# Optimization experiments

Hardware: AMD Instinct MI355X
Metric: run time of the kernel (lower is better)

## Reference

```python
import jax, jax.numpy as jnp
import numpy as np

EPS = 1e-5
B, S, P = 2, 512, 4096
TD, SD, H, ED = 512, 384, 8, 32
HD = TD // H


def _ln(x, g, b):
    m = jnp.mean(x, axis=-1, keepdims=True)
    v = jnp.var(x, axis=-1, keepdims=True)
    return (x - m) * jax.lax.rsqrt(v + EPS) * g + b


def setup_inputs() -> dict:
    key = jax.random.key(0)
    ks = iter(jax.random.split(key, 24))

    def lin(din, dout):
        W = jax.random.normal(next(ks), (din, dout), jnp.float32) / np.sqrt(din)
        b = jnp.zeros((dout,), jnp.float32)
        return W, b

    Wq, bq = lin(TD, TD)
    Wk, bk = lin(SD, TD)
    Wv, bv = lin(SD, TD)
    Wo, bo = lin(TD, TD)
    W1, b1 = lin(TD, 4 * TD)
    W2, b2 = lin(4 * TD, TD)
    edge_emb = jax.random.normal(next(ks), (H, ED), jnp.float32)
    ep_w = jax.random.normal(next(ks), (ED,), jnp.float32) / np.sqrt(ED)
    ep_b = jnp.zeros((), jnp.float32)

    return dict(
        text_features=jax.random.normal(next(ks), (B, S, TD), jnp.float32),
        shape_features=jax.random.normal(next(ks), (B, P, SD), jnp.float32),
        tn_g=jnp.ones((TD,), jnp.float32), tn_b=jnp.zeros((TD,), jnp.float32),
        sn_g=jnp.ones((SD,), jnp.float32), sn_b=jnp.zeros((SD,), jnp.float32),
        Wq=Wq, bq=bq, Wk=Wk, bk=bk, Wv=Wv, bv=bv,
        edge_emb=edge_emb, ep_w=ep_w, ep_b=ep_b,
        Wo=Wo, bo=bo,
        on_g=jnp.ones((TD,), jnp.float32), on_b=jnp.zeros((TD,), jnp.float32),
        W1=W1, b1=b1, W2=W2, b2=b2,
        fn_g=jnp.ones((TD,), jnp.float32), fn_b=jnp.zeros((TD,), jnp.float32),
    )


def reference(text_features, shape_features, tn_g, tn_b, sn_g, sn_b,
              Wq, bq, Wk, bk, Wv, bv, edge_emb, ep_w, ep_b, Wo, bo,
              on_g, on_b, W1, b1, W2, b2, fn_g, fn_b):
    b, n, _ = text_features.shape
    tn = _ln(text_features, tn_g, tn_b)
    sn = _ln(shape_features, sn_g, sn_b)
    residual = text_features

    # [b, h, n, d] projections
    q = (tn @ Wq + bq).reshape(b, n, H, HD).transpose(0, 2, 1, 3)
    k = (sn @ Wk + bk).reshape(b, -1, H, HD).transpose(0, 2, 1, 3)
    v = (sn @ Wv + bv).reshape(b, -1, H, HD).transpose(0, 2, 1, 3)

    scale = HD ** -0.5
    base_attn = jnp.einsum('bhid,bhjd->bhij', q, k) * scale  # [b,h,n,p]

    # edge_attn[:,h] = base_attn[:,h,:,:,None] * edge_emb[h]; then Linear(ED,1)+LeakyReLU.
    # Algebraically: score = leaky_relu(base_attn * (edge_emb @ ep_w) + ep_b)
    s = edge_emb @ ep_w  # [H] per-head scalar
    edge_scores = jax.nn.leaky_relu(base_attn * s[None, :, None, None] + ep_b, 0.2)

    attn = jax.nn.softmax(base_attn + edge_scores, axis=-1)
    out = jnp.einsum('bhij,bhjd->bhid', attn, v)
    out = out.transpose(0, 2, 1, 3).reshape(b, n, TD)
    out = out @ Wo + bo
    out = _ln(residual + out, on_g, on_b)

    ffn = jax.nn.gelu(out @ W1 + b1, approximate=False) @ W2 + b2
    out = _ln(out + ffn, fn_g, fn_b)
    return out, attn
```

## Files before the change

kernel.cpp:

```cpp
#include <hip/hip_runtime.h>
#include <math.h>

#define B_  2
#define S_  512
#define P_  4096
#define TD_ 512
#define SD_ 384
#define H_  8
#define HD_ 64
#define FF_ 2048

typedef _Float16 half8 __attribute__((ext_vector_type(8)));
typedef _Float16 half4 __attribute__((ext_vector_type(4)));
typedef float floatx4 __attribute__((ext_vector_type(4)));

__global__ __launch_bounds__(256) void wtrans_kernel(
    const float* __restrict__ src, _Float16* __restrict__ dst, int K, int N)
{
    __shared__ float ts[32][33];
    int k0 = blockIdx.y * 32, n0 = blockIdx.x * 32;
    int tid = threadIdx.x;
#pragma unroll
    for (int i = 0; i < 4; ++i) {
        int e = i * 256 + tid;
        int kk = e >> 5, nn = e & 31;
        ts[kk][nn] = src[(size_t)(k0 + kk) * N + n0 + nn];
    }
    __syncthreads();
#pragma unroll
    for (int i = 0; i < 4; ++i) {
        int e = i * 256 + tid;
        int nn = e >> 5, kk = e & 31;
        dst[(size_t)(n0 + nn) * K + k0 + kk] = (_Float16)ts[kk][nn];
    }
}

__device__ __forceinline__ float2 block_sum2(float a, float b) {
    for (int off = 32; off > 0; off >>= 1) {
        a += __shfl_down(a, off);
        b += __shfl_down(b, off);
    }
    __shared__ float sa[8], sb[8];
    int w = threadIdx.x >> 6;
    if ((threadIdx.x & 63) == 0) { sa[w] = a; sb[w] = b; }
    __syncthreads();
    int nw = blockDim.x >> 6;
    float ta = 0.f, tb = 0.f;
    for (int i = 0; i < nw; ++i) { ta += sa[i]; tb += sb[i]; }
    __syncthreads();
    return make_float2(ta, tb);
}

__global__ __launch_bounds__(256) void ln_in_f16_kernel(
    const float* __restrict__ x, const float* __restrict__ g,
    const float* __restrict__ be, _Float16* __restrict__ yh, int D)
{
    int row = blockIdx.x;
    const float* xr = x + (size_t)row * D;
    float s = 0.f, s2 = 0.f;
    for (int i = threadIdx.x; i < D; i += 256) {
        float v = xr[i]; s += v; s2 += v * v;
    }
    float2 r = block_sum2(s, s2);
    float mean = r.x / (float)D;
    float var  = r.y / (float)D - mean * mean;
    float rstd = rsqrtf(var + 1e-5f);
    _Float16* yr = yh + (size_t)row * D;
    for (int i = threadIdx.x; i < D; i += 256)
        yr[i] = (_Float16)((xr[i] - mean) * rstd * g[i] + be[i]);
}

__global__ __launch_bounds__(256) void ln_add_kernel(
    const float* __restrict__ a, const float* __restrict__ c,
    const float* __restrict__ g, const float* __restrict__ be,
    float* __restrict__ yf, _Float16* __restrict__ yh, int D)
{
    int row = blockIdx.x;
    const float* ar = a + (size_t)row * D;
    const float* cr = c + (size_t)row * D;
    float s = 0.f, s2 = 0.f;
    for (int i = threadIdx.x; i < D; i += 256) {
        float v = ar[i] + cr[i]; s += v; s2 += v * v;
    }
    float2 rd = block_sum2(s, s2);
    float mean = rd.x / (float)D;
    float var  = rd.y / (float)D - mean * mean;
    float rstd = rsqrtf(var + 1e-5f);
    for (int i = threadIdx.x; i < D; i += 256) {
        float v = ar[i] + cr[i];
        float o = (v - mean) * rstd * g[i] + be[i];
        if (yf) yf[(size_t)row * D + i] = o;
        if (yh) yh[(size_t)row * D + i] = (_Float16)o;
    }
}

template<int ACT, int OUTF, int OUTH, int VT>
__global__ __launch_bounds__(256) void gemm_f16_kernel(
    const _Float16* __restrict__ A, const _Float16* __restrict__ Bt,
    const float* __restrict__ bias, float* __restrict__ Cf,
    _Float16* __restrict__ Ch, int M, int N, int K)
{
    __shared__ _Float16 As[128 * 40];
    __shared__ _Float16 Bs[128 * 40];
    int tid = threadIdx.x;
    int bm = blockIdx.y * 128, bn = blockIdx.x * 128;
    int wave = tid >> 6, lane = tid & 63, quad = lane >> 4, r = lane & 15;
    int mh = (wave & 1) * 64, nh = (wave >> 1) * 64;

    floatx4 acc[4][4];
    floatx4 zz = {0.f, 0.f, 0.f, 0.f};
#pragma unroll
    for (int i = 0; i < 4; ++i)
#pragma unroll
        for (int j = 0; j < 4; ++j) acc[i][j] = zz;

    int srow = tid >> 2;
    int sko  = (tid & 3) * 8;

    for (int k0 = 0; k0 < K; k0 += 32) {
#pragma unroll
        for (int i = 0; i < 2; ++i) {
            int row = i * 64 + srow;
            *(half8*)&As[row * 40 + sko] = *(const half8*)(A  + (size_t)(bm + row) * K + k0 + sko);
            *(half8*)&Bs[row * 40 + sko] = *(const half8*)(Bt + (size_t)(bn + row) * K + k0 + sko);
        }
        __syncthreads();
        half8 af[4], bf[4];
#pragma unroll
        for (int t = 0; t < 4; ++t) {
            af[t] = *(const half8*)&As[(mh + t * 16 + r) * 40 + quad * 8];
            bf[t] = *(const half8*)&Bs[(nh + t * 16 + r) * 40 + quad * 8];
        }
#pragma unroll
        for (int i = 0; i < 4; ++i)
#pragma unroll
            for (int j = 0; j < 4; ++j)
                acc[i][j] = __builtin_amdgcn_mfma_f32_16x16x32_f16(af[i], bf[j], acc[i][j], 0, 0, 0);
        __syncthreads();
    }

#pragma unroll
    for (int j = 0; j < 4; ++j) {
        int col = bn + nh + j * 16 + r;
        float bv = bias[col];
#pragma unroll
        for (int i = 0; i < 4; ++i) {
#pragma unroll
            for (int g = 0; g < 4; ++g) {
                int row = bm + mh + i * 16 + quad * 4 + g;
                float v = acc[i][j][g] + bv;
                if (ACT) v = 0.5f * v * (1.0f + erff(v * 0.70710678118654752f));
                if (OUTF) Cf[(size_t)row * N + col] = v;
                if (OUTH) Ch[(size_t)row * N + col] = (_Float16)v;
                if (VT) {
                    int bb = row >> 12, pp = row & 4095;
                    int hh = col >> 6,  dd = col & 63;
                    Ch[((size_t)((bb * 8 + hh) * 64 + dd)) * 4096 + pp] = (_Float16)v;
                }
            }
        }
    }
}

__global__ __launch_bounds__(256) void score_stats_kernel(
    const _Float16* __restrict__ Qh, const _Float16* __restrict__ Kh,
    const float* __restrict__ edge_emb, const float* __restrict__ ep_w,
    const float* __restrict__ ep_b, float2* __restrict__ part)
{
    __shared__ _Float16 Qs[128 * 72];
    __shared__ _Float16 Ks[128 * 72];
    __shared__ float mred[2][128];
    __shared__ float sred[2][128];
    int p0 = blockIdx.x * 128, s0 = blockIdx.y * 128;
    int bh = blockIdx.z, h = bh & 7, b = bh >> 3;
    int tid = threadIdx.x;
    int wave = tid >> 6, lane = tid & 63, quad = lane >> 4, r = lane & 15;
    int mh = (wave & 1) * 64, nh = (wave >> 1) * 64;

#pragma unroll
    for (int i = 0; i < 4; ++i) {
        int row = i * 32 + (tid >> 3);
        int ko  = (tid & 7) * 8;
        *(half8*)&Qs[row * 72 + ko] = *(const half8*)(Qh + (size_t)(b * S_ + s0 + row) * TD_ + h * HD_ + ko);
        *(half8*)&Ks[row * 72 + ko] = *(const half8*)(Kh + (size_t)(b * P_ + p0 + row) * TD_ + h * HD_ + ko);
    }
    float s_h = 0.f;
#pragma unroll
    for (int e = 0; e < 32; ++e) s_h += edge_emb[h * 32 + e] * ep_w[e];
    float epbv = ep_b[0];
    __syncthreads();

    floatx4 acc[4][4];
    floatx4 zz = {0.f, 0.f, 0.f, 0.f};
#pragma unroll
    for (int i = 0; i < 4; ++i)
#pragma unroll
        for (int j = 0; j < 4; ++j) acc[i][j] = zz;

#pragma unroll
    for (int c = 0; c < 2; ++c) {
        half8 af[4], bf[4];
#pragma unroll
        for (int t = 0; t < 4; ++t) {
            af[t] = *(const half8*)&Qs[(mh + t * 16 + r) * 72 + c * 32 + quad * 8];
            bf[t] = *(const half8*)&Ks[(nh + t * 16 + r) * 72 + c * 32 + quad * 8];
        }
#pragma unroll
        for (int i = 0; i < 4; ++i)
#pragma unroll
            for (int j = 0; j < 4; ++j)
                acc[i][j] = __builtin_amdgcn_mfma_f32_16x16x32_f16(af[i], bf[j], acc[i][j], 0, 0, 0);
    }

    const float scale = 0.125f;
#pragma unroll
    for (int i = 0; i < 4; ++i)
#pragma unroll
        for (int j = 0; j < 4; ++j)
#pragma unroll
            for (int g = 0; g < 4; ++g) {
                float base = acc[i][j][g] * scale;
                float t = fmaf(base, s_h, epbv);
                float e = (t >= 0.f) ? t : 0.2f * t;
                acc[i][j][g] = base + e;
            }

    float mv[16], sv[16];
#pragma unroll
    for (int i = 0; i < 4; ++i)
#pragma unroll
        for (int g = 0; g < 4; ++g)
            mv[i * 4 + g] = fmaxf(fmaxf(acc[i][0][g], acc[i][1][g]),
                                  fmaxf(acc[i][2][g], acc[i][3][g]));
#pragma unroll
    for (int mask = 1; mask <= 8; mask <<= 1)
#pragma unroll
        for (int t = 0; t < 16; ++t)
            mv[t] = fmaxf(mv[t], __shfl_xor(mv[t], mask));
#pragma unroll
    for (int i = 0; i < 4; ++i)
#pragma unroll
        for (int g = 0; g < 4; ++g) {
            float s = 0.f;
#pragma unroll
            for (int j = 0; j < 4; ++j) s += __expf(acc[i][j][g] - mv[i * 4 + g]);
            sv[i * 4 + g] = s;
        }
#pragma unroll
    for (int mask = 1; mask <= 8; mask <<= 1)
#pragma unroll
        for (int t = 0; t < 16; ++t)
            sv[t] += __shfl_xor(sv[t], mask);

    if (r == 0) {
#pragma unroll
        for (int i = 0; i < 4; ++i)
#pragma unroll
            for (int g = 0; g < 4; ++g) {
                int row = mh + i * 16 + quad * 4 + g;
                mred[wave >> 1][row] = mv[i * 4 + g];
                sred[wave >> 1][row] = sv[i * 4 + g];
            }
    }
    __syncthreads();
    if (tid < 128) {
        float m0 = mred[0][tid], m1 = mred[1][tid];
        float m = fmaxf(m0, m1);
        float s = sred[0][tid] * __expf(m0 - m) + sred[1][tid] * __expf(m1 - m);
        part[(size_t)blockIdx.x * (B_ * H_ * S_) + (size_t)bh * S_ + s0 + tid] = make_float2(m, s);
    }
}

__global__ __launch_bounds__(256) void rowstats_kernel(
    const float2* __restrict__ part, float2* __restrict__ rs)
{
    int row = blockIdx.x * 256 + threadIdx.x;
    float2 v = part[row];
    float m = v.x, l = v.y;
#pragma unroll
    for (int t = 1; t < 32; ++t) {
        float2 p = part[(size_t)t * (B_ * H_ * S_) + row];
        float nm = fmaxf(m, p.x);
        l = l * __expf(m - nm) + p.y * __expf(p.x - nm);
        m = nm;
    }
    rs[row] = make_float2(m, 1.0f / l);
}

__global__ __launch_bounds__(256) void zero_kernel(float4* __restrict__ p, int n4)
{
    int i = blockIdx.x * 256 + threadIdx.x;
    if (i < n4) p[i] = make_float4(0.f, 0.f, 0.f, 0.f);
}

__global__ __launch_bounds__(256) void attn_pv_kernel(
    const _Float16* __restrict__ Qh, const _Float16* __restrict__ Kh,
    const _Float16* __restrict__ Vt,
    const float* __restrict__ edge_emb, const float* __restrict__ ep_w,
    const float* __restrict__ ep_b, const float2* __restrict__ rowstats,
    float* __restrict__ attn, float* __restrict__ ctx_f32)
{
    __shared__ _Float16 Qs[32 * 72];
    __shared__ _Float16 Ks[128 * 72];
    __shared__ _Float16 Vs[64 * 136];
    __shared__ _Float16 As[32 * 136];
    __shared__ float2 ms_sh[32];

    int s0 = blockIdx.x * 32;
    int split = blockIdx.y;
    int bh = blockIdx.z, h = bh & 7, b = bh >> 3;
    int tid = threadIdx.x;
    int wave = tid >> 6, lane = tid & 63, quad = lane >> 4, r = lane & 15;

    {
        int row = tid >> 3, ko = (tid & 7) * 8;
        *(half8*)&Qs[row * 72 + ko] =
            *(const half8*)(Qh + (size_t)(b * S_ + s0 + row) * TD_ + h * HD_ + ko);
    }
    if (tid < 32) ms_sh[tid] = rowstats[bh * S_ + s0 + tid];

    float s_h = 0.f;
#pragma unroll
    for (int e = 0; e < 32; ++e) s_h += edge_emb[h * 32 + e] * ep_w[e];
    float epbv = ep_b[0];

    floatx4 zz = {0.f, 0.f, 0.f, 0.f};
    floatx4 accpv[2];
    accpv[0] = zz; accpv[1] = zz;

    for (int pc = 0; pc < 1024; pc += 128) {
        int pg = split * 1024 + pc;
        __syncthreads();
#pragma unroll
        for (int ii = 0; ii < 4; ++ii) {
            int e = ii * 256 + tid;
            int row = e >> 3, ko = (e & 7) * 8;
            *(half8*)&Ks[row * 72 + ko] =
                *(const half8*)(Kh + (size_t)(b * P_ + pg + row) * TD_ + h * HD_ + ko);
        }
#pragma unroll
        for (int ii = 0; ii < 4; ++ii) {
            int e = ii * 256 + tid;
            int row = e >> 4, po = (e & 15) * 8;
            *(half8*)&Vs[row * 136 + po] =
                *(const half8*)(Vt + ((size_t)bh * 64 + row) * (size_t)P_ + pg + po);
        }
        __syncthreads();

        floatx4 accs[2][2];
        accs[0][0] = zz; accs[0][1] = zz; accs[1][0] = zz; accs[1][1] = zz;
#pragma unroll
        for (int c = 0; c < 2; ++c) {
            half8 aq[2], bk[2];
#pragma unroll
            for (int i = 0; i < 2; ++i)
                aq[i] = *(const half8*)&Qs[(i * 16 + r) * 72 + c * 32 + quad * 8];
#pragma unroll
            for (int j = 0; j < 2; ++j)
                bk[j] = *(const half8*)&Ks[(wave * 32 + j * 16 + r) * 72 + c * 32 + quad * 8];
#pragma unroll
            for (int i = 0; i < 2; ++i)
#pragma unroll
                for (int j = 0; j < 2; ++j)
                    accs[i][j] = __builtin_amdgcn_mfma_f32_16x16x32_f16(aq[i], bk[j], accs[i][j], 0, 0, 0);
        }

        const float scale = 0.125f;
#pragma unroll
        for (int i = 0; i < 2; ++i)
#pragma unroll
            for (int j = 0; j < 2; ++j) {
                int colp = wave * 32 + j * 16 + r;
#pragma unroll
                for (int g = 0; g < 4; ++g) {
                    int srow = i * 16 + quad * 4 + g;
                    float base = accs[i][j][g] * scale;
                    float t = fmaf(base, s_h, epbv);
                    float e = (t >= 0.f) ? t : 0.2f * t;
                    float z = base + e;
                    float2 ms = ms_sh[srow];
                    float p = __expf(z - ms.x) * ms.y;
                    attn[((size_t)bh * S_ + s0 + srow) * P_ + pg + colp] = p;
                    As[srow * 136 + colp] = (_Float16)p;
                }
            }
        __syncthreads();

#pragma unroll
        for (int c = 0; c < 4; ++c) {
            half8 bv = *(const half8*)&Vs[(wave * 16 + r) * 136 + c * 32 + quad * 8];
#pragma unroll
            for (int i2 = 0; i2 < 2; ++i2) {
                half8 ap = *(const half8*)&As[(i2 * 16 + r) * 136 + c * 32 + quad * 8];
                accpv[i2] = __builtin_amdgcn_mfma_f32_16x16x32_f16(ap, bv, accpv[i2], 0, 0, 0);
            }
        }
    }

#pragma unroll
    for (int i2 = 0; i2 < 2; ++i2)
#pragma unroll
        for (int g = 0; g < 4; ++g) {
            int srow = s0 + i2 * 16 + quad * 4 + g;
            int d = wave * 16 + r;
            atomicAdd(&ctx_f32[(size_t)(b * S_ + srow) * TD_ + h * HD_ + d], accpv[i2][g]);
        }
}

__global__ __launch_bounds__(256) void cast_ctx_kernel(
    const float4* __restrict__ src, _Float16* __restrict__ dst, int n4)
{
    int i = blockIdx.x * 256 + threadIdx.x;
    if (i < n4) {
        float4 v = src[i];
        half4 hv = { (_Float16)v.x, (_Float16)v.y, (_Float16)v.z, (_Float16)v.w };
        *(half4*)&dst[(size_t)i * 4] = hv;
    }
}

extern "C" void kernel_launch(void* const* d_in, const int* in_sizes, int n_in,
                              void* d_out, int out_size, void* d_ws, size_t ws_size,
                              hipStream_t stream) {
    const float* text  = (const float*)d_in[0];
    const float* shape = (const float*)d_in[1];
    const float* tn_g  = (const float*)d_in[2];
    const float* tn_b  = (const float*)d_in[3];
    const float* sn_g  = (const float*)d_in[4];
    const float* sn_b  = (const float*)d_in[5];
    const float* Wq    = (const float*)d_in[6];
    const float* bq    = (const float*)d_in[7];
    const float* Wk    = (const float*)d_in[8];
    const float* bk    = (const float*)d_in[9];
    const float* Wv    = (const float*)d_in[10];
    const float* bv    = (const float*)d_in[11];
    const float* edge  = (const float*)d_in[12];
    const float* epw   = (const float*)d_in[13];
    const float* epb   = (const float*)d_in[14];
    const float* Wo    = (const float*)d_in[15];
    const float* bo    = (const float*)d_in[16];
    const float* on_g  = (const float*)d_in[17];
    const float* on_b  = (const float*)d_in[18];
    const float* W1    = (const float*)d_in[19];
    const float* b1    = (const float*)d_in[20];
    const float* W2    = (const float*)d_in[21];
    const float* b2    = (const float*)d_in[22];
    const float* fn_g  = (const float*)d_in[23];
    const float* fn_b  = (const float*)d_in[24];

    float* out_f  = (float*)d_out;
    float* attn_f = out_f + (size_t)B_ * S_ * TD_;

    char* w = (char*)d_ws;
    _Float16* tn_h   = (_Float16*)w; w += (size_t)1024 * 512 * 2;
    _Float16* sn_h   = (_Float16*)w; w += (size_t)8192 * 384 * 2;
    _Float16* Q_h    = (_Float16*)w; w += (size_t)1024 * 512 * 2;
    _Float16* K_h    = (_Float16*)w; w += (size_t)8192 * 512 * 2;
    _Float16* Vt_h   = (_Float16*)w; w += (size_t)16 * 64 * 4096 * 2;
    _Float16* ctx_h  = (_Float16*)w; w += (size_t)1024 * 512 * 2;
    _Float16* out1_h = (_Float16*)w; w += (size_t)1024 * 512 * 2;
    _Float16* h1_h   = (_Float16*)w; w += (size_t)1024 * 2048 * 2;
    _Float16* Wqt    = (_Float16*)w; w += (size_t)512 * 512 * 2;
    _Float16* Wkt    = (_Float16*)w; w += (size_t)512 * 384 * 2;
    _Float16* Wvt    = (_Float16*)w; w += (size_t)512 * 384 * 2;
    _Float16* Wot    = (_Float16*)w; w += (size_t)512 * 512 * 2;
    _Float16* W1t    = (_Float16*)w; w += (size_t)2048 * 512 * 2;
    _Float16* W2t    = (_Float16*)w; w += (size_t)512 * 2048 * 2;
    float*    tmp    = (float*)w;    w += (size_t)1024 * 512 * 4;
    float*    out1_f = (float*)w;    w += (size_t)1024 * 512 * 4;

    float2* part     = (float2*)sn_h;
    float2* rowstats = part + (size_t)32 * 8192;
    float*  ctx_f32  = tmp;

    wtrans_kernel<<<dim3(16, 16), 256, 0, stream>>>(Wq, Wqt, 512, 512);
    wtrans_kernel<<<dim3(16, 12), 256, 0, stream>>>(Wk, Wkt, 384, 512);
    wtrans_kernel<<<dim3(16, 12), 256, 0, stream>>>(Wv, Wvt, 384, 512);
    wtrans_kernel<<<dim3(16, 16), 256, 0, stream>>>(Wo, Wot, 512, 512);
    wtrans_kernel<<<dim3(64, 16), 256, 0, stream>>>(W1, W1t, 512, 2048);
    wtrans_kernel<<<dim3(16, 64), 256, 0, stream>>>(W2, W2t, 2048, 512);

    ln_in_f16_kernel<<<B_ * S_, 256, 0, stream>>>(text, tn_g, tn_b, tn_h, TD_);
    ln_in_f16_kernel<<<B_ * P_, 256, 0, stream>>>(shape, sn_g, sn_b, sn_h, SD_);

    gemm_f16_kernel<0,0,1,0><<<dim3(4, 8),  256, 0, stream>>>(tn_h, Wqt, bq, nullptr, Q_h, 1024, 512, 512);
    gemm_f16_kernel<0,0,1,0><<<dim3(4, 64), 256, 0, stream>>>(sn_h, Wkt, bk, nullptr, K_h, 8192, 512, 384);
    gemm_f16_kernel<0,0,0,1><<<dim3(4, 64), 256, 0, stream>>>(sn_h, Wvt, bv, nullptr, Vt_h, 8192, 512, 384);

    score_stats_kernel<<<dim3(P_ / 128, S_ / 128, B_ * H_), 256, 0, stream>>>(
        Q_h, K_h, edge, epw, epb, part);
    rowstats_kernel<<<dim3(32), 256, 0, stream>>>(part, rowstats);
    zero_kernel<<<dim3(512), 256, 0, stream>>>((float4*)ctx_f32, 131072);
    attn_pv_kernel<<<dim3(S_ / 32, 4, B_ * H_), 256, 0, stream>>>(
        Q_h, K_h, Vt_h, edge, epw, epb, rowstats, attn_f, ctx_f32);
    cast_ctx_kernel<<<dim3(512), 256, 0, stream>>>((const float4*)ctx_f32, ctx_h, 131072);

    gemm_f16_kernel<0,1,0,0><<<dim3(4, 8), 256, 0, stream>>>(ctx_h, Wot, bo, tmp, nullptr, 1024, 512, 512);
    ln_add_kernel<<<B_ * S_, 256, 0, stream>>>(text, tmp, on_g, on_b, out1_f, out1_h, TD_);

    gemm_f16_kernel<1,0,1,0><<<dim3(16, 8), 256, 0, stream>>>(out1_h, W1t, b1, nullptr, h1_h, 1024, 2048, 512);
    gemm_f16_kernel<0,1,0,0><<<dim3(4, 8),  256, 0, stream>>>(h1_h, W2t, b2, tmp, nullptr, 1024, 512, 2048);
    ln_add_kernel<<<B_ * S_, 256, 0, stream>>>(out1_f, tmp, fn_g, fn_b, out_f, nullptr, TD_);
}
```

Measured before the change: 411.1 us.

## Merge small launches, fold rowstats into attn, split-K W2 GEMM, drop ctx atomics

Merges the six weight transposes into one launch, the two input layernorms into one, and the Q/K/V projections into a single GEMM launch. The rowstats reduction moves into attn_pv_kernel. The ctx atomicAdds are replaced by per-split partial buffers summed in a cast kernel, which removes the zero kernel. The W2 GEMM uses 4-way split-K with partials summed inside the final layernorm. This cuts launch count and atomic traffic and gives the under-occupied W2 GEMM more blocks, at the cost of extra partial-buffer memory traffic and redundant rowstats recomputation in every attn block.

After: 366.8 us. -10.8%, faster.

```diff
diff --git a/kernel.cpp b/kernel.cpp
--- a/kernel.cpp
+++ b/kernel.cpp
@@ -14,11 +14,25 @@
 typedef _Float16 half4 __attribute__((ext_vector_type(4)));
 typedef float floatx4 __attribute__((ext_vector_type(4)));
 
-__global__ __launch_bounds__(256) void wtrans_kernel(
-    const float* __restrict__ src, _Float16* __restrict__ dst, int K, int N)
+__global__ __launch_bounds__(256) void wtrans_all_kernel(
+    const float* __restrict__ s0p, const float* __restrict__ s1p,
+    const float* __restrict__ s2p, const float* __restrict__ s3p,
+    const float* __restrict__ s4p, const float* __restrict__ s5p,
+    _Float16* __restrict__ d0p, _Float16* __restrict__ d1p,
+    _Float16* __restrict__ d2p, _Float16* __restrict__ d3p,
+    _Float16* __restrict__ d4p, _Float16* __restrict__ d5p)
 {
     __shared__ float ts[32][33];
-    int k0 = blockIdx.y * 32, n0 = blockIdx.x * 32;
+    int id = blockIdx.x;
+    const float* src; _Float16* dst; int K, N, t, nlog;
+    if (id < 256)       { src=s0p; dst=d0p; K=512;  N=512;  t=id;       nlog=4; }
+    else if (id < 448)  { src=s1p; dst=d1p; K=384;  N=512;  t=id-256;   nlog=4; }
+    else if (id < 640)  { src=s2p; dst=d2p; K=384;  N=512;  t=id-448;   nlog=4; }
+    else if (id < 896)  { src=s3p; dst=d3p; K=512;  N=512;  t=id-640;   nlog=4; }
+    else if (id < 1920) { src=s4p; dst=d4p; K=512;  N=2048; t=id-896;   nlog=6; }
+    else                { src=s5p; dst=d5p; K=2048; N=512;  t=id-1920;  nlog=4; }
+    int n0 = (t & ((1 << nlog) - 1)) << 5;
+    int k0 = (t >> nlog) << 5;
     int tid = threadIdx.x;
 #pragma unroll
     for (int i = 0; i < 4; ++i) {
@@ -51,12 +65,22 @@
     return make_float2(ta, tb);
 }
 
-__global__ __launch_bounds__(256) void ln_in_f16_kernel(
-    const float* __restrict__ x, const float* __restrict__ g,
-    const float* __restrict__ be, _Float16* __restrict__ yh, int D)
+__global__ __launch_bounds__(256) void ln_both_kernel(
+    const float* __restrict__ text, const float* __restrict__ shape,
+    const float* __restrict__ tn_g, const float* __restrict__ tn_b,
+    const float* __restrict__ sn_g, const float* __restrict__ sn_b,
+    _Float16* __restrict__ tn_h, _Float16* __restrict__ sn_h)
 {
     int row = blockIdx.x;
-    const float* xr = x + (size_t)row * D;
+    const float* xr; const float* g; const float* be; _Float16* yr; int D;
+    if (row < 1024) {
+        D = 512; xr = text + (size_t)row * 512; g = tn_g; be = tn_b;
+        yr = tn_h + (size_t)row * 512;
+    } else {
+        int r2 = row - 1024;
+        D = 384; xr = shape + (size_t)r2 * 384; g = sn_g; be = sn_b;
+        yr = sn_h + (size_t)r2 * 384;
+    }
     float s = 0.f, s2 = 0.f;
     for (int i = threadIdx.x; i < D; i += 256) {
         float v = xr[i]; s += v; s2 += v * v;
@@ -65,13 +89,12 @@
     float mean = r.x / (float)D;
     float var  = r.y / (float)D - mean * mean;
     float rstd = rsqrtf(var + 1e-5f);
-    _Float16* yr = yh + (size_t)row * D;
     for (int i = threadIdx.x; i < D; i += 256)
         yr[i] = (_Float16)((xr[i] - mean) * rstd * g[i] + be[i]);
 }
 
 __global__ __launch_bounds__(256) void ln_add_kernel(
-    const float* __restrict__ a, const float* __restrict__ c,
+    const float* __restrict__ a, const float* __restrict__ c, int np, int cstride,
     const float* __restrict__ g, const float* __restrict__ be,
     float* __restrict__ yf, _Float16* __restrict__ yh, int D)
 {
@@ -80,21 +103,24 @@
     const float* cr = c + (size_t)row * D;
     float s = 0.f, s2 = 0.f;
     for (int i = threadIdx.x; i < D; i += 256) {
-        float v = ar[i] + cr[i]; s += v; s2 += v * v;
+        float v = ar[i];
+        for (int t = 0; t < np; ++t) v += cr[(size_t)t * cstride + i];
+        s += v; s2 += v * v;
     }
     float2 rd = block_sum2(s, s2);
     float mean = rd.x / (float)D;
     float var  = rd.y / (float)D - mean * mean;
     float rstd = rsqrtf(var + 1e-5f);
     for (int i = threadIdx.x; i < D; i += 256) {
-        float v = ar[i] + cr[i];
+        float v = ar[i];
+        for (int t = 0; t < np; ++t) v += cr[(size_t)t * cstride + i];
         float o = (v - mean) * rstd * g[i] + be[i];
         if (yf) yf[(size_t)row * D + i] = o;
         if (yh) yh[(size_t)row * D + i] = (_Float16)o;
     }
 }
 
-template<int ACT, int OUTF, int OUTH, int VT>
+template<int ACT, int OUTF, int OUTH, int SPLITK>
 __global__ __launch_bounds__(256) void gemm_f16_kernel(
     const _Float16* __restrict__ A, const _Float16* __restrict__ Bt,
     const float* __restrict__ bias, float* __restrict__ Cf,
@@ -117,7 +143,11 @@
     int srow = tid >> 2;
     int sko  = (tid & 3) * 8;
 
-    for (int k0 = 0; k0 < K; k0 += 32) {
+    int ksplit = (SPLITK > 1) ? blockIdx.z : 0;
+    int kbeg = ksplit * (K / SPLITK);
+    int kend = kbeg + K / SPLITK;
+
+    for (int k0 = kbeg; k0 < kend; k0 += 32) {
 #pragma unroll
         for (int i = 0; i < 2; ++i) {
             int row = i * 64 + srow;
@@ -142,7 +172,7 @@
 #pragma unroll
     for (int j = 0; j < 4; ++j) {
         int col = bn + nh + j * 16 + r;
-        float bv = bias[col];
+        float bv = (SPLITK == 1 || ksplit == 0) ? bias[col] : 0.f;
 #pragma unroll
         for (int i = 0; i < 4; ++i) {
 #pragma unroll
@@ -150,12 +180,82 @@
                 int row = bm + mh + i * 16 + quad * 4 + g;
                 float v = acc[i][j][g] + bv;
                 if (ACT) v = 0.5f * v * (1.0f + erff(v * 0.70710678118654752f));
-                if (OUTF) Cf[(size_t)row * N + col] = v;
+                if (OUTF) Cf[(size_t)ksplit * M * N + (size_t)row * N + col] = v;
                 if (OUTH) Ch[(size_t)row * N + col] = (_Float16)v;
-                if (VT) {
+            }
+        }
+    }
+}
+
+__global__ __launch_bounds__(256) void qkv_gemm_kernel(
+    const _Float16* __restrict__ tn, const _Float16* __restrict__ sn,
+    const _Float16* __restrict__ Wqt, const _Float16* __restrict__ Wkt,
+    const _Float16* __restrict__ Wvt,
+    const float* __restrict__ bq, const float* __restrict__ bk,
+    const float* __restrict__ bv,
+    _Float16* __restrict__ Qh, _Float16* __restrict__ Kh, _Float16* __restrict__ Vth)
+{
+    __shared__ _Float16 As[128 * 40];
+    __shared__ _Float16 Bs[128 * 40];
+    int by = blockIdx.y;
+    const _Float16* A; const _Float16* Bt; const float* bias; _Float16* out;
+    int K, bm, vt;
+    if (by < 8)       { A = tn; Bt = Wqt; bias = bq; K = 512; bm = by * 128;        vt = 0; out = Qh;  }
+    else if (by < 72) { A = sn; Bt = Wkt; bias = bk; K = 384; bm = (by - 8) * 128;  vt = 0; out = Kh;  }
+    else              { A = sn; Bt = Wvt; bias = bv; K = 384; bm = (by - 72) * 128; vt = 1; out = Vth; }
+    int bn = blockIdx.x * 128;
+    int tid = threadIdx.x;
+    int wave = tid >> 6, lane = tid & 63, quad = lane >> 4, r = lane & 15;
+    int mh = (wave & 1) * 64, nh = (wave >> 1) * 64;
+
+    floatx4 acc[4][4];
+    floatx4 zz = {0.f, 0.f, 0.f, 0.f};
+#pragma unroll
+    for (int i = 0; i < 4; ++i)
+#pragma unroll
+        for (int j = 0; j < 4; ++j) acc[i][j] = zz;
+
+    int srow = tid >> 2;
+    int sko  = (tid & 3) * 8;
+
+    for (int k0 = 0; k0 < K; k0 += 32) {
+#pragma unroll
+        for (int i = 0; i < 2; ++i) {
+            int row = i * 64 + srow;
+            *(half8*)&As[row * 40 + sko] = *(const half8*)(A  + (size_t)(bm + row) * K + k0 + sko);
+            *(half8*)&Bs[row * 40 + sko] = *(const half8*)(Bt + (size_t)(bn + row) * K + k0 + sko);
+        }
+        __syncthreads();
+        half8 af[4], bf[4];
+#pragma unroll
+        for (int t = 0; t < 4; ++t) {
+            af[t] = *(const half8*)&As[(mh + t * 16 + r) * 40 + quad * 8];
+            bf[t] = *(const half8*)&Bs[(nh + t * 16 + r) * 40 + quad * 8];
+        }
+#pragma unroll
+        for (int i = 0; i < 4; ++i)
+#pragma unroll
+            for (int j = 0; j < 4; ++j)
+                acc[i][j] = __builtin_amdgcn_mfma_f32_16x16x32_f16(af[i], bf[j], acc[i][j], 0, 0, 0);
+        __syncthreads();
+    }
+
+#pragma unroll
+    for (int j = 0; j < 4; ++j) {
+        int col = bn + nh + j * 16 + r;
+        float bvv = bias[col];
+#pragma unroll
+        for (int i = 0; i < 4; ++i) {
+#pragma unroll
+            for (int g = 0; g < 4; ++g) {
+                int row = bm + mh + i * 16 + quad * 4 + g;
+                float v = acc[i][j][g] + bvv;
+                if (!vt) {
+                    out[(size_t)row * 512 + col] = (_Float16)v;
+                } else {
                     int bb = row >> 12, pp = row & 4095;
                     int hh = col >> 6,  dd = col & 63;
-                    Ch[((size_t)((bb * 8 + hh) * 64 + dd)) * 4096 + pp] = (_Float16)v;
+                    out[((size_t)((bb * 8 + hh) * 64 + dd)) * 4096 + pp] = (_Float16)v;
                 }
             }
         }
@@ -271,34 +371,12 @@
     }
 }
 
-__global__ __launch_bounds__(256) void rowstats_kernel(
-    const float2* __restrict__ part, float2* __restrict__ rs)
-{
-    int row = blockIdx.x * 256 + threadIdx.x;
-    float2 v = part[row];
-    float m = v.x, l = v.y;
-#pragma unroll
-    for (int t = 1; t < 32; ++t) {
-        float2 p = part[(size_t)t * (B_ * H_ * S_) + row];
-        float nm = fmaxf(m, p.x);
-        l = l * __expf(m - nm) + p.y * __expf(p.x - nm);
-        m = nm;
-    }
-    rs[row] = make_float2(m, 1.0f / l);
-}
-
-__global__ __launch_bounds__(256) void zero_kernel(float4* __restrict__ p, int n4)
-{
-    int i = blockIdx.x * 256 + threadIdx.x;
-    if (i < n4) p[i] = make_float4(0.f, 0.f, 0.f, 0.f);
-}
-
 __global__ __launch_bounds__(256) void attn_pv_kernel(
     const _Float16* __restrict__ Qh, const _Float16* __restrict__ Kh,
     const _Float16* __restrict__ Vt,
     const float* __restrict__ edge_emb, const float* __restrict__ ep_w,
-    const float* __restrict__ ep_b, const float2* __restrict__ rowstats,
-    float* __restrict__ attn, float* __restrict__ ctx_f32)
+    const float* __restrict__ ep_b, const float2* __restrict__ part,
+    float* __restrict__ attn, float* __restrict__ ctx_part)
 {
     __shared__ _Float16 Qs[32 * 72];
     __shared__ _Float16 Ks[128 * 72];
@@ -317,7 +395,19 @@
         *(half8*)&Qs[row * 72 + ko] =
             *(const half8*)(Qh + (size_t)(b * S_ + s0 + row) * TD_ + h * HD_ + ko);
     }
-    if (tid < 32) ms_sh[tid] = rowstats[bh * S_ + s0 + tid];
+    if (tid < 32) {
+        int base = bh * S_ + s0 + tid;
+        float2 v = part[base];
+        float m = v.x, l = v.y;
+#pragma unroll
+        for (int t = 1; t < 32; ++t) {
+            float2 p = part[(size_t)t * (B_ * H_ * S_) + base];
+            float nm = fmaxf(m, p.x);
+            l = l * __expf(m - nm) + p.y * __expf(p.x - nm);
+            m = nm;
+        }
+        ms_sh[tid] = make_float2(m, 1.0f / l);
+    }
 
     float s_h = 0.f;
 #pragma unroll
@@ -397,22 +487,28 @@
         }
     }
 
+    float* dst = ctx_part + (size_t)split * (1024 * 512);
 #pragma unroll
     for (int i2 = 0; i2 < 2; ++i2)
 #pragma unroll
         for (int g = 0; g < 4; ++g) {
             int srow = s0 + i2 * 16 + quad * 4 + g;
             int d = wave * 16 + r;
-            atomicAdd(&ctx_f32[(size_t)(b * S_ + srow) * TD_ + h * HD_ + d], accpv[i2][g]);
-        }
-}
-
-__global__ __launch_bounds__(256) void cast_ctx_kernel(
+            dst[(size_t)(b * S_ + srow) * TD_ + h * HD_ + d] = accpv[i2][g];
+        }
+}
+
+__global__ __launch_bounds__(256) void sumcast_kernel(
     const float4* __restrict__ src, _Float16* __restrict__ dst, int n4)
 {
     int i = blockIdx.x * 256 + threadIdx.x;
     if (i < n4) {
-        float4 v = src[i];
+        float4 a = src[i];
+        float4 bq = src[i + 131072];
+        float4 c = src[i + 262144];
+        float4 d = src[i + 393216];
+        float4 v = make_float4(a.x + bq.x + c.x + d.x, a.y + bq.y + c.y + d.y,
+                               a.z + bq.z + c.z + d.z, a.w + bq.w + c.w + d.w);
         half4 hv = { (_Float16)v.x, (_Float16)v.y, (_Float16)v.z, (_Float16)v.w };
         *(half4*)&dst[(size_t)i * 4] = hv;
     }
@@ -467,37 +563,28 @@
     _Float16* W2t    = (_Float16*)w; w += (size_t)512 * 2048 * 2;
     float*    tmp    = (float*)w;    w += (size_t)1024 * 512 * 4;
     float*    out1_f = (float*)w;    w += (size_t)1024 * 512 * 4;
-
-    float2* part     = (float2*)sn_h;
-    float2* rowstats = part + (size_t)32 * 8192;
-    float*  ctx_f32  = tmp;
-
-    wtrans_kernel<<<dim3(16, 16), 256, 0, stream>>>(Wq, Wqt, 512, 512);
-    wtrans_kernel<<<dim3(16, 12), 256, 0, stream>>>(Wk, Wkt, 384, 512);
-    wtrans_kernel<<<dim3(16, 12), 256, 0, stream>>>(Wv, Wvt, 384, 512);
-    wtrans_kernel<<<dim3(16, 16), 256, 0, stream>>>(Wo, Wot, 512, 512);
-    wtrans_kernel<<<dim3(64, 16), 256, 0, stream>>>(W1, W1t, 512, 2048);
-    wtrans_kernel<<<dim3(16, 64), 256, 0, stream>>>(W2, W2t, 2048, 512);
-
-    ln_in_f16_kernel<<<B_ * S_, 256, 0, stream>>>(text, tn_g, tn_b, tn_h, TD_);
-    ln_in_f16_kernel<<<B_ * P_, 256, 0, stream>>>(shape, sn_g, sn_b, sn_h, SD_);
-
-    gemm_f16_kernel<0,0,1,0><<<dim3(4, 8),  256, 0, stream>>>(tn_h, Wqt, bq, nullptr, Q_h, 1024, 512, 512);
-    gemm_f16_kernel<0,0,1,0><<<dim3(4, 64), 256, 0, stream>>>(sn_h, Wkt, bk, nullptr, K_h, 8192, 512, 384);
-    gemm_f16_kernel<0,0,0,1><<<dim3(4, 64), 256, 0, stream>>>(sn_h, Wvt, bv, nullptr, Vt_h, 8192, 512, 384);
+    float*    ctx_part = (float*)w;  w += (size_t)4 * 1024 * 512 * 4;
+
+    float2* part = (float2*)sn_h;
+
+    wtrans_all_kernel<<<2944, 256, 0, stream>>>(Wq, Wk, Wv, Wo, W1, W2,
+                                                Wqt, Wkt, Wvt, Wot, W1t, W2t);
+
+    ln_both_kernel<<<1024 + 8192, 256, 0, stream>>>(text, shape, tn_g, tn_b, sn_g, sn_b, tn_h, sn_h);
+
+    qkv_gemm_kernel<<<dim3(4, 136), 256, 0, stream>>>(tn_h, sn_h, Wqt, Wkt, Wvt,
+                                                      bq, bk, bv, Q_h, K_h, Vt_h);
 
     score_stats_kernel<<<dim3(P_ / 128, S_ / 128, B_ * H_), 256, 0, stream>>>(
         Q_h, K_h, edge, epw, epb, part);
-    rowstats_kernel<<<dim3(32), 256, 0, stream>>>(part, rowstats);
-    zero_kernel<<<dim3(512), 256, 0, stream>>>((float4*)ctx_f32, 131072);
     attn_pv_kernel<<<dim3(S_ / 32, 4, B_ * H_), 256, 0, stream>>>(
-        Q_h, K_h, Vt_h, edge, epw, epb, rowstats, attn_f, ctx_f32);
-    cast_ctx_kernel<<<dim3(512), 256, 0, stream>>>((const float4*)ctx_f32, ctx_h, 131072);
-
-    gemm_f16_kernel<0,1,0,0><<<dim3(4, 8), 256, 0, stream>>>(ctx_h, Wot, bo, tmp, nullptr, 1024, 512, 512);
-    ln_add_kernel<<<B_ * S_, 256, 0, stream>>>(text, tmp, on_g, on_b, out1_f, out1_h, TD_);
-
-    gemm_f16_kernel<1,0,1,0><<<dim3(16, 8), 256, 0, stream>>>(out1_h, W1t, b1, nullptr, h1_h, 1024, 2048, 512);
-    gemm_f16_kernel<0,1,0,0><<<dim3(4, 8),  256, 0, stream>>>(h1_h, W2t, b2, tmp, nullptr, 1024, 512, 2048);
-    ln_add_kernel<<<B_ * S_, 256, 0, stream>>>(out1_f, tmp, fn_g, fn_b, out_f, nullptr, TD_);
-}
+        Q_h, K_h, Vt_h, edge, epw, epb, part, attn_f, ctx_part);
+    sumcast_kernel<<<dim3(512), 256, 0, stream>>>((const float4*)ctx_part, ctx_h, 131072);
+
+    gemm_f16_kernel<0,1,0,1><<<dim3(4, 8), 256, 0, stream>>>(ctx_h, Wot, bo, tmp, nullptr, 1024, 512, 512);
+    ln_add_kernel<<<B_ * S_, 256, 0, stream>>>(text, tmp, 1, 0, on_g, on_b, out1_f, out1_h, TD_);
+
+    gemm_f16_kernel<1,0,1,1><<<dim3(16, 8), 256, 0, stream>>>(out1_h, W1t, b1, nullptr, h1_h, 1024, 2048, 512);
+    gemm_f16_kernel<0,1,0,4><<<dim3(4, 8, 4), 256, 0, stream>>>(h1_h, W2t, b2, ctx_part, nullptr, 1024, 512, 2048);
+    ln_add_kernel<<<B_ * S_, 256, 0, stream>>>(out1_f, ctx_part, 4, 1024 * 512, fn_g, fn_b, out_f, nullptr, TD_);
+}
```
